# Kernel optimization log

Hardware: AMD Instinct MI355X
Metric: run time of the kernel (lower is better)

## Reference

```python
import jax, jax.numpy as jnp
import numpy as np

B, D, E, C = 16384, 2048, 16, 64  # batch, feat_dim, num_experts, classes per expert
CLASS_STARTS = np.arange(E, dtype=np.int32) * C  # contiguous equal-size class ranges


def setup_inputs() -> dict:
    key = jax.random.key(0)
    k1, k2, k3, k4, k5 = jax.random.split(key, 5)
    return {
        "features": jax.random.normal(k1, (B, D), dtype=jnp.float32),
        "coarse_w": jax.random.normal(k2, (E, D), dtype=jnp.float32) * 0.02,
        "coarse_b": jax.random.normal(k3, (E,), dtype=jnp.float32) * 0.02,
        "expert_w": jax.random.normal(k4, (E, C, D), dtype=jnp.float32) * 0.02,
        "expert_b": jax.random.normal(k5, (E, C), dtype=jnp.float32) * 0.02,
    }


def reference(features, coarse_w, coarse_b, expert_w, expert_b):
    # coarse router: Linear(feat_dim -> num_experts)
    coarse_output = features @ coarse_w.T + coarse_b          # [B, E]
    expert_id = jnp.argmax(coarse_output, axis=1)             # [B] top-1 routing

    # all-expert heads as one batched GEMM, then select routed expert per sample
    # (same math as gather-by-mask + per-expert Linear + scatter-back loop)
    y_all = jnp.einsum('bd,ecd->bec', features, expert_w) + expert_b  # [B, E, C]
    y = jnp.take_along_axis(y_all, expert_id[:, None, None], axis=1)[:, 0, :]  # [B, C]

    # local_preds: softmax probs of the routed expert (all experts have C = max classes)
    local_preds = jax.nn.softmax(y, axis=1)                   # [B, C]

    # global prediction = local argmax + expert's class-range start
    starts = jnp.asarray(CLASS_STARTS)
    global_preds = (jnp.argmax(y, axis=1) + starts[expert_id]).astype(jnp.float32)  # [B]

    return coarse_output, expert_id, local_preds, global_preds
```

## Files before the change

kernel.cpp:

```cpp
#include <hip/hip_runtime.h>
#include <cstdint>

typedef _Float16 f16;
typedef f16 f16x8 __attribute__((ext_vector_type(8)));
typedef float f32x4 __attribute__((ext_vector_type(4)));
#define MFMA16(a, b, c) __builtin_amdgcn_mfma_f32_16x16x32_f16((a), (b), (c), 0, 0, 0)

static constexpr int B_ = 16384;
static constexpr int D_ = 2048;
static constexpr int E_ = 16;
static constexpr int C_ = 64;
static constexpr float LSC = 2048.0f;
static constexpr float ILSC = 1.0f / 2048.0f;
static constexpr int TR_E = 128;
static constexpr int SK_E = 8;
static constexpr int MAXITEMS = (B_ / TR_E) + E_;

__device__ __forceinline__ void cvt_hl(const float4 x, const float4 y,
                                       f16x8& h, f16x8& l) {
  const float av[8] = {x.x, x.y, x.z, x.w, y.x, y.y, y.z, y.w};
#pragma unroll
  for (int j = 0; j < 8; ++j) {
    const f16 hh = (f16)av[j];
    h[j] = hh;
    l[j] = (f16)((av[j] - (float)hh) * LSC);
  }
}

__global__ __launch_bounds__(256) void convert_w(
    const float* __restrict__ cw, const float* __restrict__ ew,
    f16* __restrict__ cwH, f16* __restrict__ cwL,
    f16* __restrict__ ewH, f16* __restrict__ ewL) {
  const int g = blockIdx.x;
  const int tid = threadIdx.x;
  const float* src;
  f16 *dh, *dl;
  size_t off;
  if (g < 16) {
    off = ((size_t)g * 256 + tid) * 8;
    src = cw; dh = cwH; dl = cwL;
  } else {
    off = ((size_t)(g - 16) * 256 + tid) * 8;
    src = ew; dh = ewH; dl = ewL;
  }
  const float4 v0 = *(const float4*)(src + off);
  const float4 v1 = *(const float4*)(src + off + 4);
  f16x8 h8, l8;
  cvt_hl(v0, v1, h8, l8);
  *(f16x8*)(dh + off) = h8;
  *(f16x8*)(dl + off) = l8;
}

__global__ __launch_bounds__(512) void coarse_fused(
    const float* __restrict__ feat, const f16* __restrict__ cwH,
    const f16* __restrict__ cwL, const float* __restrict__ cb,
    float* __restrict__ out0, float* __restrict__ out1,
    int* __restrict__ eidArr) {
  __shared__ float red[8 * 256];
  const int tid = threadIdx.x;
  const int w = tid >> 6;
  const int lane = tid & 63;
  const int rl = lane & 15;
  const int kq = lane >> 4;
  const int row = blockIdx.x * 16 + rl;
  const int k0 = w * (D_ / 8);

  const float* fr = feat + (size_t)row * D_ + k0 + kq * 8;
  const f16* bhp = cwH + (size_t)rl * D_ + k0 + kq * 8;
  const f16* blp = cwL + (size_t)rl * D_ + k0 + kq * 8;

  f32x4 aH = {0.f, 0.f, 0.f, 0.f};
  f32x4 aC = {0.f, 0.f, 0.f, 0.f};

  float4 v0 = *(const float4*)(fr);
  float4 v1 = *(const float4*)(fr + 4);
  f16x8 bhn = *(const f16x8*)(bhp);
  f16x8 bln = *(const f16x8*)(blp);
#pragma unroll
  for (int ch = 0; ch < 8; ++ch) {
    const float4 c0 = v0, c1 = v1;
    const f16x8 bh = bhn, bl = bln;
    if (ch + 1 < 8) {
      const int ko = (ch + 1) * 32;
      v0 = *(const float4*)(fr + ko);
      v1 = *(const float4*)(fr + ko + 4);
      bhn = *(const f16x8*)(bhp + ko);
      bln = *(const f16x8*)(blp + ko);
    }
    f16x8 h8, l8;
    cvt_hl(c0, c1, h8, l8);
    aH = MFMA16(h8, bh, aH);
    aC = MFMA16(h8, bl, aC);
    aC = MFMA16(l8, bh, aC);
  }
#pragma unroll
  for (int reg = 0; reg < 4; ++reg)
    red[w * 256 + (kq * 4 + reg) * 16 + rl] = aH[reg] + aC[reg] * ILSC;
  __syncthreads();

  if (tid < 256) {
    const int e = tid & 15;
    const int lrow = tid >> 4;
    float val = cb[e];
#pragma unroll
    for (int ww = 0; ww < 8; ++ww) val += red[ww * 256 + tid];
    const int grow = blockIdx.x * 16 + lrow;
    out0[(size_t)grow * E_ + e] = val;
    float av2 = val;
    int ai = e;
#pragma unroll
    for (int off = 8; off; off >>= 1) {
      const float ov = __shfl_xor(av2, off, 16);
      const int oi = __shfl_xor(ai, off, 16);
      if (ov > av2 || (ov == av2 && oi < ai)) { av2 = ov; ai = oi; }
    }
    if (e == 0) {
      out1[grow] = (float)ai;
      eidArr[grow] = ai;
    }
  }
}

__global__ __launch_bounds__(256) void route_build(
    const int* __restrict__ eidArr, int* __restrict__ cnt,
    int* __restrict__ rowList) {
  __shared__ int lcnt[E_];
  __shared__ int lbase[E_];
  const int tid = threadIdx.x;
  if (tid < E_) lcnt[tid] = 0;
  __syncthreads();
  const int row = blockIdx.x * 256 + tid;
  const int best = eidArr[row];
  const int lpos = atomicAdd(&lcnt[best], 1);
  __syncthreads();
  if (tid < E_) lbase[tid] = atomicAdd(&cnt[tid], lcnt[tid]);
  __syncthreads();
  rowList[best * B_ + lbase[best] + lpos] = row;
}

__global__ void make_schedule(const int* __restrict__ cnt,
                              int* __restrict__ sched,
                              int* __restrict__ nItems) {
  __shared__ int tiles[E_];
  __shared__ int offs[E_];
  const int t = threadIdx.x;
  if (t < E_) tiles[t] = (cnt[t] + TR_E - 1) / TR_E;
  __syncthreads();
  if (t == 0) {
    int acc = 0;
    for (int e = 0; e < E_; ++e) { offs[e] = acc; acc += tiles[e]; }
    *nItems = acc;
  }
  __syncthreads();
  if (t < E_) {
    const int o = offs[t], n = tiles[t];
    for (int k = 0; k < n; ++k) sched[o + k] = t | (k << 8);
  }
}

__global__ __launch_bounds__(256) void expert_gemm(
    const float* __restrict__ feat,
    const f16* __restrict__ ewH, const f16* __restrict__ ewL,
    const int* __restrict__ rowList, const int* __restrict__ cnt,
    const int* __restrict__ sched, const int* __restrict__ nItems,
    float* __restrict__ part0, float* __restrict__ partRest) {
  __shared__ int rIdx[TR_E];
  const int b = blockIdx.x;
  const int kz = b % SK_E;
  const int item = b / SK_E;
  if (item >= *nItems) return;
  const int s = sched[item];
  const int e = s & 255;
  const int tile = s >> 8;
  const int count = cnt[e];

  const int tid = threadIdx.x;
  if (tid < TR_E) {
    const int slot = tile * TR_E + tid;
    rIdx[tid] = (slot < count) ? rowList[e * B_ + slot] : 0;
  }
  __syncthreads();

  const int lane = tid & 63;
  const int w = tid >> 6;
  const int rl = lane & 15;
  const int kq = lane >> 4;

  const int grow0 = rIdx[w * 32 + rl];
  const int grow1 = rIdx[w * 32 + 16 + rl];
  constexpr int KRANGE = D_ / SK_E;
  constexpr int NCH = KRANGE / 32;
  const int k0 = kz * KRANGE;

  const float* pa0 = feat + (size_t)grow0 * D_ + k0 + kq * 8;
  const float* pa1 = feat + (size_t)grow1 * D_ + k0 + kq * 8;
  const size_t eoff = (size_t)e * C_ * D_;
  const f16* pbh[4];
  const f16* pbl[4];
#pragma unroll
  for (int ct = 0; ct < 4; ++ct) {
    const size_t co = eoff + (size_t)(ct * 16 + rl) * D_ + k0 + kq * 8;
    pbh[ct] = ewH + co;
    pbl[ct] = ewL + co;
  }

  f32x4 accH[2][4], accC[2][4];
#pragma unroll
  for (int s2 = 0; s2 < 2; ++s2)
#pragma unroll
    for (int ct = 0; ct < 4; ++ct) {
      accH[s2][ct] = (f32x4){0.f, 0.f, 0.f, 0.f};
      accC[s2][ct] = (f32x4){0.f, 0.f, 0.f, 0.f};
    }

  float4 n0a = *(const float4*)(pa0);
  float4 n0b = *(const float4*)(pa0 + 4);
  float4 n1a = *(const float4*)(pa1);
  float4 n1b = *(const float4*)(pa1 + 4);
#pragma unroll
  for (int ch = 0; ch < NCH; ++ch) {
    const float4 c0a = n0a, c0b = n0b, c1a = n1a, c1b = n1b;
    if (ch + 1 < NCH) {
      const int kn = (ch + 1) * 32;
      n0a = *(const float4*)(pa0 + kn);
      n0b = *(const float4*)(pa0 + kn + 4);
      n1a = *(const float4*)(pa1 + kn);
      n1b = *(const float4*)(pa1 + kn + 4);
    }
    f16x8 a0h, a0l, a1h, a1l;
    cvt_hl(c0a, c0b, a0h, a0l);
    cvt_hl(c1a, c1b, a1h, a1l);
    const int ko = ch * 32;
#pragma unroll
    for (int ct = 0; ct < 4; ++ct) {
      const f16x8 bh = *(const f16x8*)(pbh[ct] + ko);
      const f16x8 bl = *(const f16x8*)(pbl[ct] + ko);
      accH[0][ct] = MFMA16(a0h, bh, accH[0][ct]);
      accC[0][ct] = MFMA16(a0h, bl, accC[0][ct]);
      accC[0][ct] = MFMA16(a0l, bh, accC[0][ct]);
      accH[1][ct] = MFMA16(a1h, bh, accH[1][ct]);
      accC[1][ct] = MFMA16(a1h, bl, accC[1][ct]);
      accC[1][ct] = MFMA16(a1l, bh, accC[1][ct]);
    }
  }

  float* pk = kz ? (partRest + (size_t)(kz - 1) * B_ * C_) : part0;
#pragma unroll
  for (int s2 = 0; s2 < 2; ++s2)
#pragma unroll
    for (int reg = 0; reg < 4; ++reg) {
      const int rloc = w * 32 + s2 * 16 + kq * 4 + reg;
      const int slot = tile * TR_E + rloc;
      if (slot < count) {
        const int g = rIdx[rloc];
#pragma unroll
        for (int ct = 0; ct < 4; ++ct)
          pk[(size_t)g * C_ + ct * 16 + rl] =
              accH[s2][ct][reg] + accC[s2][ct][reg] * ILSC;
      }
    }
}

template <int SK>
__global__ __launch_bounds__(256) void finish_rows(
    const float* __restrict__ ypart0, const float* __restrict__ ypartRest,
    const float* __restrict__ eb, const int* __restrict__ eidArr,
    float* __restrict__ out2, float* __restrict__ out3) {
  const int lane = threadIdx.x & 63;
  const int row = (blockIdx.x * 256 + threadIdx.x) >> 6;
  const int eid = eidArr[row];

  float v = eb[eid * C_ + lane];
  v += ypart0[(size_t)row * C_ + lane];
#pragma unroll
  for (int kz = 1; kz < SK; ++kz)
    v += ypartRest[((size_t)(kz - 1) * B_ + row) * C_ + lane];

  float m = v;
#pragma unroll
  for (int off = 32; off; off >>= 1) m = fmaxf(m, __shfl_xor(m, off, 64));
  const float p = __expf(v - m);
  float s = p;
#pragma unroll
  for (int off = 32; off; off >>= 1) s += __shfl_xor(s, off, 64);
  out2[(size_t)row * C_ + lane] = p / s;

  float av = v;
  int ai = lane;
#pragma unroll
  for (int off = 32; off; off >>= 1) {
    const float ov = __shfl_xor(av, off, 64);
    const int oi = __shfl_xor(ai, off, 64);
    if (ov > av || (ov == av && oi < ai)) { av = ov; ai = oi; }
  }
  if (lane == 0) out3[row] = (float)(ai + (eid << 6));
}

extern "C" void kernel_launch(void* const* d_in, const int* in_sizes, int n_in,
                              void* d_out, int out_size, void* d_ws,
                              size_t ws_size, hipStream_t stream) {
  const float* feat = (const float*)d_in[0];
  const float* cw = (const float*)d_in[1];
  const float* cb = (const float*)d_in[2];
  const float* ew = (const float*)d_in[3];
  const float* eb = (const float*)d_in[4];

  float* out0 = (float*)d_out;
  float* out1 = out0 + (size_t)B_ * E_;
  float* out2 = out1 + B_;
  float* out3 = out2 + (size_t)B_ * C_;

  char* p = (char*)d_ws;
  f16* ewH = (f16*)p;        p += (size_t)E_ * C_ * D_ * 2;
  f16* ewL = (f16*)p;        p += (size_t)E_ * C_ * D_ * 2;
  f16* cwH = (f16*)p;        p += (size_t)E_ * D_ * 2;
  f16* cwL = (f16*)p;        p += (size_t)E_ * D_ * 2;
  float* ypartRest = (float*)p; p += (size_t)(SK_E - 1) * B_ * C_ * 4;
  int* rowList = (int*)p;    p += (size_t)E_ * B_ * 4;
  int* cnt = (int*)p;        p += 64 * 4;
  int* eidArr = (int*)p;     p += (size_t)B_ * 4;
  int* sched = (int*)p;      p += 512 * 4;
  int* nItems = (int*)p;

  hipMemsetAsync(cnt, 0, E_ * sizeof(int), stream);

  convert_w<<<16 + 1024, 256, 0, stream>>>(cw, ew, cwH, cwL, ewH, ewL);
  coarse_fused<<<B_ / 16, 512, 0, stream>>>(feat, cwH, cwL, cb, out0, out1,
                                            eidArr);
  route_build<<<B_ / 256, 256, 0, stream>>>(eidArr, cnt, rowList);
  make_schedule<<<1, 64, 0, stream>>>(cnt, sched, nItems);
  expert_gemm<<<MAXITEMS * SK_E, 256, 0, stream>>>(
      feat, ewH, ewL, rowList, cnt, sched, nItems, out2, ypartRest);
  finish_rows<SK_E><<<(B_ * 64) / 256, 256, 0, stream>>>(out2, ypartRest, eb,
                                                         eidArr, out2, out3);
}
```

Baseline: 283.2 us.

## Fuse schedule build into route_build and prefetch expert weights in GEMM

```diff
diff --git a/kernel.cpp b/kernel.cpp
--- a/kernel.cpp
+++ b/kernel.cpp
@@ -123,9 +123,13 @@
 
 __global__ __launch_bounds__(256) void route_build(
     const int* __restrict__ eidArr, int* __restrict__ cnt,
-    int* __restrict__ rowList) {
+    int* __restrict__ rowList, int* __restrict__ sched,
+    int* __restrict__ nItems, int* __restrict__ doneCnt) {
   __shared__ int lcnt[E_];
   __shared__ int lbase[E_];
+  __shared__ int tiles[E_];
+  __shared__ int offs[E_];
+  __shared__ int isLast;
   const int tid = threadIdx.x;
   if (tid < E_) lcnt[tid] = 0;
   __syncthreads();
@@ -136,25 +140,28 @@
   if (tid < E_) lbase[tid] = atomicAdd(&cnt[tid], lcnt[tid]);
   __syncthreads();
   rowList[best * B_ + lbase[best] + lpos] = row;
-}
-
-__global__ void make_schedule(const int* __restrict__ cnt,
-                              int* __restrict__ sched,
-                              int* __restrict__ nItems) {
-  __shared__ int tiles[E_];
-  __shared__ int offs[E_];
-  const int t = threadIdx.x;
-  if (t < E_) tiles[t] = (cnt[t] + TR_E - 1) / TR_E;
-  __syncthreads();
-  if (t == 0) {
-    int acc = 0;
-    for (int e = 0; e < E_; ++e) { offs[e] = acc; acc += tiles[e]; }
-    *nItems = acc;
-  }
-  __syncthreads();
-  if (t < E_) {
-    const int o = offs[t], n = tiles[t];
-    for (int k = 0; k < n; ++k) sched[o + k] = t | (k << 8);
+
+  __syncthreads();
+  if (tid == 0) {
+    __threadfence();
+    const int d = atomicAdd(doneCnt, 1);
+    isLast = (d == (int)gridDim.x - 1) ? 1 : 0;
+  }
+  __syncthreads();
+  if (isLast) {
+    if (tid < E_)
+      tiles[tid] = (atomicAdd(&cnt[tid], 0) + TR_E - 1) / TR_E;
+    __syncthreads();
+    if (tid == 0) {
+      int acc = 0;
+      for (int e2 = 0; e2 < E_; ++e2) { offs[e2] = acc; acc += tiles[e2]; }
+      *nItems = acc;
+    }
+    __syncthreads();
+    if (tid < E_) {
+      const int o = offs[tid], n = tiles[tid];
+      for (int k = 0; k < n; ++k) sched[o + k] = tid | (k << 8);
+    }
   }
 }
 
@@ -217,30 +224,41 @@
   float4 n0b = *(const float4*)(pa0 + 4);
   float4 n1a = *(const float4*)(pa1);
   float4 n1b = *(const float4*)(pa1 + 4);
+  f16x8 bhn[4], bln[4];
+#pragma unroll
+  for (int ct = 0; ct < 4; ++ct) {
+    bhn[ct] = *(const f16x8*)(pbh[ct]);
+    bln[ct] = *(const f16x8*)(pbl[ct]);
+  }
 #pragma unroll
   for (int ch = 0; ch < NCH; ++ch) {
     const float4 c0a = n0a, c0b = n0b, c1a = n1a, c1b = n1b;
+    f16x8 bhc[4], blc[4];
+#pragma unroll
+    for (int ct = 0; ct < 4; ++ct) { bhc[ct] = bhn[ct]; blc[ct] = bln[ct]; }
     if (ch + 1 < NCH) {
       const int kn = (ch + 1) * 32;
       n0a = *(const float4*)(pa0 + kn);
       n0b = *(const float4*)(pa0 + kn + 4);
       n1a = *(const float4*)(pa1 + kn);
       n1b = *(const float4*)(pa1 + kn + 4);
+#pragma unroll
+      for (int ct = 0; ct < 4; ++ct) {
+        bhn[ct] = *(const f16x8*)(pbh[ct] + kn);
+        bln[ct] = *(const f16x8*)(pbl[ct] + kn);
+      }
     }
     f16x8 a0h, a0l, a1h, a1l;
     cvt_hl(c0a, c0b, a0h, a0l);
     cvt_hl(c1a, c1b, a1h, a1l);
-    const int ko = ch * 32;
 #pragma unroll
     for (int ct = 0; ct < 4; ++ct) {
-      const f16x8 bh = *(const f16x8*)(pbh[ct] + ko);
-      const f16x8 bl = *(const f16x8*)(pbl[ct] + ko);
-      accH[0][ct] = MFMA16(a0h, bh, accH[0][ct]);
-      accC[0][ct] = MFMA16(a0h, bl, accC[0][ct]);
-      accC[0][ct] = MFMA16(a0l, bh, accC[0][ct]);
-      accH[1][ct] = MFMA16(a1h, bh, accH[1][ct]);
-      accC[1][ct] = MFMA16(a1h, bl, accC[1][ct]);
-      accC[1][ct] = MFMA16(a1l, bh, accC[1][ct]);
+      accH[0][ct] = MFMA16(a0h, bhc[ct], accH[0][ct]);
+      accC[0][ct] = MFMA16(a0h, blc[ct], accC[0][ct]);
+      accC[0][ct] = MFMA16(a0l, bhc[ct], accC[0][ct]);
+      accH[1][ct] = MFMA16(a1h, bhc[ct], accH[1][ct]);
+      accC[1][ct] = MFMA16(a1h, blc[ct], accC[1][ct]);
+      accC[1][ct] = MFMA16(a1l, bhc[ct], accC[1][ct]);
     }
   }
 
@@ -321,14 +339,15 @@
   int* eidArr = (int*)p;     p += (size_t)B_ * 4;
   int* sched = (int*)p;      p += 512 * 4;
   int* nItems = (int*)p;
-
-  hipMemsetAsync(cnt, 0, E_ * sizeof(int), stream);
+  int* doneCnt = cnt + 16;
+
+  hipMemsetAsync(cnt, 0, 32 * sizeof(int), stream);
 
   convert_w<<<16 + 1024, 256, 0, stream>>>(cw, ew, cwH, cwL, ewH, ewL);
   coarse_fused<<<B_ / 16, 512, 0, stream>>>(feat, cwH, cwL, cb, out0, out1,
                                             eidArr);
-  route_build<<<B_ / 256, 256, 0, stream>>>(eidArr, cnt, rowList);
-  make_schedule<<<1, 64, 0, stream>>>(cnt, sched, nItems);
+  route_build<<<B_ / 256, 256, 0, stream>>>(eidArr, cnt, rowList, sched,
+                                            nItems, doneCnt);
   expert_gemm<<<MAXITEMS * SK_E, 256, 0, stream>>>(
       feat, ewH, ewL, rowList, cnt, sched, nItems, out2, ypartRest);
   finish_rows<SK_E><<<(B_ * 64) / 256, 256, 0, stream>>>(out2, ypartRest, eb,
```

After: 290.1 us. +2.4%, slower.

## Pre-pack split-f16 weights into MFMA fragment order for coalesced loads

Applied to the files above, without the earlier changes.

```diff
diff --git a/kernel.cpp b/kernel.cpp
--- a/kernel.cpp
+++ b/kernel.cpp
@@ -14,6 +14,7 @@
 static constexpr float ILSC = 1.0f / 2048.0f;
 static constexpr int TR_E = 128;
 static constexpr int SK_E = 8;
+static constexpr int NCHG = D_ / 32;
 static constexpr int MAXITEMS = (B_ / TR_E) + E_;
 
 __device__ __forceinline__ void cvt_hl(const float4 x, const float4 y,
@@ -27,33 +28,45 @@
   }
 }
 
-__global__ __launch_bounds__(256) void convert_w(
+__global__ __launch_bounds__(256) void convert_pack(
     const float* __restrict__ cw, const float* __restrict__ ew,
-    f16* __restrict__ cwH, f16* __restrict__ cwL,
-    f16* __restrict__ ewH, f16* __restrict__ ewL) {
+    f16* __restrict__ cwPH, f16* __restrict__ cwPL,
+    f16* __restrict__ ewPH, f16* __restrict__ ewPL) {
   const int g = blockIdx.x;
   const int tid = threadIdx.x;
-  const float* src;
-  f16 *dh, *dl;
-  size_t off;
   if (g < 16) {
-    off = ((size_t)g * 256 + tid) * 8;
-    src = cw; dh = cwH; dl = cwL;
+    const int t = g * 256 + tid;
+    const int ch = t >> 6;
+    const int lane = t & 63;
+    const int rl = lane & 15, kq = lane >> 4;
+    const float* src = cw + (size_t)rl * D_ + ch * 32 + kq * 8;
+    const float4 v0 = *(const float4*)src;
+    const float4 v1 = *(const float4*)(src + 4);
+    f16x8 h8, l8;
+    cvt_hl(v0, v1, h8, l8);
+    *(f16x8*)(cwPH + (size_t)t * 8) = h8;
+    *(f16x8*)(cwPL + (size_t)t * 8) = l8;
   } else {
-    off = ((size_t)(g - 16) * 256 + tid) * 8;
-    src = ew; dh = ewH; dl = ewL;
-  }
-  const float4 v0 = *(const float4*)(src + off);
-  const float4 v1 = *(const float4*)(src + off + 4);
-  f16x8 h8, l8;
-  cvt_hl(v0, v1, h8, l8);
-  *(f16x8*)(dh + off) = h8;
-  *(f16x8*)(dl + off) = l8;
-}
-
-__global__ __launch_bounds__(512) void coarse_fused(
-    const float* __restrict__ feat, const f16* __restrict__ cwH,
-    const f16* __restrict__ cwL, const float* __restrict__ cb,
+    const int t = (g - 16) * 256 + tid;
+    const int lane = t & 63;
+    const int ct = (t >> 6) & 3;
+    const int ch = (t >> 8) & 63;
+    const int e = t >> 14;
+    const int rl = lane & 15, kq = lane >> 4;
+    const float* src =
+        ew + ((size_t)e * C_ + ct * 16 + rl) * D_ + ch * 32 + kq * 8;
+    const float4 v0 = *(const float4*)src;
+    const float4 v1 = *(const float4*)(src + 4);
+    f16x8 h8, l8;
+    cvt_hl(v0, v1, h8, l8);
+    *(f16x8*)(ewPH + (size_t)t * 8) = h8;
+    *(f16x8*)(ewPL + (size_t)t * 8) = l8;
+  }
+}
+
+__global__ __launch_bounds__(512, 4) void coarse_fused(
+    const float* __restrict__ feat, const f16* __restrict__ cwPH,
+    const f16* __restrict__ cwPL, const float* __restrict__ cb,
     float* __restrict__ out0, float* __restrict__ out1,
     int* __restrict__ eidArr) {
   __shared__ float red[8 * 256];
@@ -63,35 +76,39 @@
   const int rl = lane & 15;
   const int kq = lane >> 4;
   const int row = blockIdx.x * 16 + rl;
-  const int k0 = w * (D_ / 8);
-
-  const float* fr = feat + (size_t)row * D_ + k0 + kq * 8;
-  const f16* bhp = cwH + (size_t)rl * D_ + k0 + kq * 8;
-  const f16* blp = cwL + (size_t)rl * D_ + k0 + kq * 8;
+
+  const float* fr = feat + (size_t)row * D_ + w * 256 + kq * 8;
+  const f16* pbh = cwPH + (size_t)(w * 8) * 512 + lane * 8;
+  const f16* pbl = cwPL + (size_t)(w * 8) * 512 + lane * 8;
 
   f32x4 aH = {0.f, 0.f, 0.f, 0.f};
   f32x4 aC = {0.f, 0.f, 0.f, 0.f};
 
-  float4 v0 = *(const float4*)(fr);
-  float4 v1 = *(const float4*)(fr + 4);
-  f16x8 bhn = *(const f16x8*)(bhp);
-  f16x8 bln = *(const f16x8*)(blp);
+  float4 pA[2][2];
+  pA[0][0] = *(const float4*)(fr);
+  pA[0][1] = *(const float4*)(fr + 4);
+  pA[1][0] = *(const float4*)(fr + 32);
+  pA[1][1] = *(const float4*)(fr + 36);
+  f16x8 bh = *(const f16x8*)(pbh);
+  f16x8 bl = *(const f16x8*)(pbl);
 #pragma unroll
   for (int ch = 0; ch < 8; ++ch) {
-    const float4 c0 = v0, c1 = v1;
-    const f16x8 bh = bhn, bl = bln;
+    const int cur = ch & 1;
+    const float4 c0 = pA[cur][0], c1 = pA[cur][1];
+    const f16x8 bhc = bh, blc = bl;
+    if (ch + 2 < 8) {
+      pA[cur][0] = *(const float4*)(fr + (ch + 2) * 32);
+      pA[cur][1] = *(const float4*)(fr + (ch + 2) * 32 + 4);
+    }
     if (ch + 1 < 8) {
-      const int ko = (ch + 1) * 32;
-      v0 = *(const float4*)(fr + ko);
-      v1 = *(const float4*)(fr + ko + 4);
-      bhn = *(const f16x8*)(bhp + ko);
-      bln = *(const f16x8*)(blp + ko);
+      bh = *(const f16x8*)(pbh + (ch + 1) * 512);
+      bl = *(const f16x8*)(pbl + (ch + 1) * 512);
     }
     f16x8 h8, l8;
     cvt_hl(c0, c1, h8, l8);
-    aH = MFMA16(h8, bh, aH);
-    aC = MFMA16(h8, bl, aC);
-    aC = MFMA16(l8, bh, aC);
+    aH = MFMA16(h8, bhc, aH);
+    aC = MFMA16(h8, blc, aC);
+    aC = MFMA16(l8, bhc, aC);
   }
 #pragma unroll
   for (int reg = 0; reg < 4; ++reg)
@@ -160,7 +177,7 @@
 
 __global__ __launch_bounds__(256) void expert_gemm(
     const float* __restrict__ feat,
-    const f16* __restrict__ ewH, const f16* __restrict__ ewL,
+    const f16* __restrict__ ewPH, const f16* __restrict__ ewPL,
     const int* __restrict__ rowList, const int* __restrict__ cnt,
     const int* __restrict__ sched, const int* __restrict__ nItems,
     float* __restrict__ part0, float* __restrict__ partRest) {
@@ -194,15 +211,8 @@
 
   const float* pa0 = feat + (size_t)grow0 * D_ + k0 + kq * 8;
   const float* pa1 = feat + (size_t)grow1 * D_ + k0 + kq * 8;
-  const size_t eoff = (size_t)e * C_ * D_;
-  const f16* pbh[4];
-  const f16* pbl[4];
-#pragma unroll
-  for (int ct = 0; ct < 4; ++ct) {
-    const size_t co = eoff + (size_t)(ct * 16 + rl) * D_ + k0 + kq * 8;
-    pbh[ct] = ewH + co;
-    pbl[ct] = ewL + co;
-  }
+  const f16* pbh = ewPH + ((size_t)e * NCHG + kz * 8) * 2048 + lane * 8;
+  const f16* pbl = ewPL + ((size_t)e * NCHG + kz * 8) * 2048 + lane * 8;
 
   f32x4 accH[2][4], accC[2][4];
 #pragma unroll
@@ -230,11 +240,10 @@
     f16x8 a0h, a0l, a1h, a1l;
     cvt_hl(c0a, c0b, a0h, a0l);
     cvt_hl(c1a, c1b, a1h, a1l);
-    const int ko = ch * 32;
 #pragma unroll
     for (int ct = 0; ct < 4; ++ct) {
-      const f16x8 bh = *(const f16x8*)(pbh[ct] + ko);
-      const f16x8 bl = *(const f16x8*)(pbl[ct] + ko);
+      const f16x8 bh = *(const f16x8*)(pbh + ch * 2048 + ct * 512);
+      const f16x8 bl = *(const f16x8*)(pbl + ch * 2048 + ct * 512);
       accH[0][ct] = MFMA16(a0h, bh, accH[0][ct]);
       accC[0][ct] = MFMA16(a0h, bl, accC[0][ct]);
       accC[0][ct] = MFMA16(a0l, bh, accC[0][ct]);
@@ -311,26 +320,26 @@
   float* out3 = out2 + (size_t)B_ * C_;
 
   char* p = (char*)d_ws;
-  f16* ewH = (f16*)p;        p += (size_t)E_ * C_ * D_ * 2;
-  f16* ewL = (f16*)p;        p += (size_t)E_ * C_ * D_ * 2;
-  f16* cwH = (f16*)p;        p += (size_t)E_ * D_ * 2;
-  f16* cwL = (f16*)p;        p += (size_t)E_ * D_ * 2;
+  f16* ewPH = (f16*)p;    p += (size_t)E_ * C_ * D_ * 2;
+  f16* ewPL = (f16*)p;    p += (size_t)E_ * C_ * D_ * 2;
+  f16* cwPH = (f16*)p;    p += (size_t)E_ * D_ * 2;
+  f16* cwPL = (f16*)p;    p += (size_t)E_ * D_ * 2;
   float* ypartRest = (float*)p; p += (size_t)(SK_E - 1) * B_ * C_ * 4;
-  int* rowList = (int*)p;    p += (size_t)E_ * B_ * 4;
-  int* cnt = (int*)p;        p += 64 * 4;
-  int* eidArr = (int*)p;     p += (size_t)B_ * 4;
-  int* sched = (int*)p;      p += 512 * 4;
+  int* rowList = (int*)p; p += (size_t)E_ * B_ * 4;
+  int* cnt = (int*)p;     p += 64 * 4;
+  int* eidArr = (int*)p;  p += (size_t)B_ * 4;
+  int* sched = (int*)p;   p += 512 * 4;
   int* nItems = (int*)p;
 
   hipMemsetAsync(cnt, 0, E_ * sizeof(int), stream);
 
-  convert_w<<<16 + 1024, 256, 0, stream>>>(cw, ew, cwH, cwL, ewH, ewL);
-  coarse_fused<<<B_ / 16, 512, 0, stream>>>(feat, cwH, cwL, cb, out0, out1,
+  convert_pack<<<16 + 1024, 256, 0, stream>>>(cw, ew, cwPH, cwPL, ewPH, ewPL);
+  coarse_fused<<<B_ / 16, 512, 0, stream>>>(feat, cwPH, cwPL, cb, out0, out1,
                                             eidArr);
   route_build<<<B_ / 256, 256, 0, stream>>>(eidArr, cnt, rowList);
   make_schedule<<<1, 64, 0, stream>>>(cnt, sched, nItems);
   expert_gemm<<<MAXITEMS * SK_E, 256, 0, stream>>>(
-      feat, ewH, ewL, rowList, cnt, sched, nItems, out2, ypartRest);
+      feat, ewPH, ewPL, rowList, cnt, sched, nItems, out2, ypartRest);
   finish_rows<SK_E><<<(B_ * 64) / 256, 256, 0, stream>>>(out2, ypartRest, eb,
                                                          eidArr, out2, out3);
 }
```

After: 262.5 us. 1.08x faster.
